# Optimization experiments

Measured on AMD Instinct MI355X. Metric: run time of the kernel, lower is better.

Reference implementation:

```python
import jax, jax.numpy as jnp
import numpy as np

B, TQ, TV, D = 8, 2048, 2048, 128
NEG = 1e9  # keras Attention uses additive -1e9 masking for fp32


def setup_inputs() -> dict:
    key = jax.random.key(0)
    kq, kv, kk, kmq, kmv = jax.random.split(key, 5)
    q = jax.random.normal(kq, (B, TQ, D), dtype=jnp.float32)
    v = jax.random.normal(kv, (B, TV, D), dtype=jnp.float32)
    k = jax.random.normal(kk, (B, TV, D), dtype=jnp.float32)
    # learned scalar scale from use_scale=True, initialized to ones
    scale = jnp.ones((), dtype=jnp.float32)
    mask_q = jax.random.randint(kmq, (B, TQ), 0, 2) > 0
    mask_v = jax.random.randint(kmv, (B, TV), 0, 2) > 0
    return {"q": q, "v": v, "k": k, "scale": scale, "mask_q": mask_q, "mask_v": mask_v}


def reference(q, v, k, scale, mask_q, mask_v):
    # scores: [B, Tq, Tv]
    scores = scale * jnp.einsum('bqd,bkd->bqk', q, k)
    # key/value mask: additive -1e9 on masked positions (keras semantics)
    scores = scores - NEG * (1.0 - mask_v[:, None, :].astype(scores.dtype))
    weights = jax.nn.softmax(scores, axis=-1)
    out = jnp.einsum('bqk,bkd->bqd', weights, v)
    # query mask zeroes out masked query rows
    out = out * mask_q[:, :, None].astype(out.dtype)
    return out
```

## Files before the change

### kernel.cpp

```cpp
#include <hip/hip_runtime.h>
#include <cstddef>

#define NB 8
#define TQ 2048
#define TV 2048
#define DD 128
#define KVT 32
#define NWV 4
#define CHW (TV / NWV)
#define NT  (CHW / KVT)

typedef _Float16 f16x8 __attribute__((ext_vector_type(8)));
typedef _Float16 f16x4 __attribute__((ext_vector_type(4)));
typedef float f32x4 __attribute__((ext_vector_type(4)));

template <int CTRL>
__device__ __forceinline__ float dpp_mov(float x) {
  return __builtin_bit_cast(float,
      __builtin_amdgcn_update_dpp(0, __builtin_bit_cast(int, x), CTRL, 0xF, 0xF, true));
}
__device__ __forceinline__ float rowmax16(float x) {
  x = fmaxf(x, dpp_mov<0x128>(x));
  x = fmaxf(x, dpp_mov<0x124>(x));
  x = fmaxf(x, dpp_mov<0x122>(x));
  x = fmaxf(x, dpp_mov<0x121>(x));
  return x;
}

__global__ __launch_bounds__(256) void prepass_kernel(
    const float* __restrict__ q, const float* __restrict__ k,
    const float* __restrict__ v, const float* __restrict__ scale_p,
    _Float16* __restrict__ qh, _Float16* __restrict__ kh2, _Float16* __restrict__ vt2)
{
  __shared__ _Float16 tlds[32 * 34];
  const int tid = threadIdx.x;
  const int bid = blockIdx.x;
  if (bid < 2048) {
    const float sc = scale_p[0];
    size_t idx = (size_t)bid * 256 + tid;
    float4 x = ((const float4*)q)[idx];
    f16x4 h; h[0] = (_Float16)(sc * x.x); h[1] = (_Float16)(sc * x.y);
    h[2] = (_Float16)(sc * x.z); h[3] = (_Float16)(sc * x.w);
    ((f16x4*)qh)[idx] = h;
  } else if (bid < 2048 + 512) {
    int tb = bid - 2048;
    int b = tb >> 6, kt = tb & 63;
    int row = tid >> 3, d0 = (tid & 7) * 4;
    const float* src = k + ((size_t)(b * TV + kt * 32 + row)) * DD;
    _Float16* dst = kh2 + ((size_t)(b * 64 + kt)) * 4096;
#pragma unroll
    for (int it = 0; it < 4; ++it) {
      float4 x = *(const float4*)(src + it * 32 + d0);
      f16x4 h; h[0] = (_Float16)x.x; h[1] = (_Float16)x.y;
      h[2] = (_Float16)x.z; h[3] = (_Float16)x.w;
      *(f16x4*)(dst + it * 1024 + row * 32 + d0) = h;
    }
  } else {
    int tb = bid - 2048 - 512;
    int b = tb >> 8, rem = tb & 255;
    int kt = rem >> 2, dt = rem & 3;
    int r = tid >> 3, c0 = (tid & 7) * 4;
    float4 x = *(const float4*)&v[((size_t)b * TV + kt * 32 + r) * DD + dt * 32 + c0];
    tlds[(c0 + 0) * 34 + r] = (_Float16)x.x;
    tlds[(c0 + 1) * 34 + r] = (_Float16)x.y;
    tlds[(c0 + 2) * 34 + r] = (_Float16)x.z;
    tlds[(c0 + 3) * 34 + r] = (_Float16)x.w;
    __syncthreads();
    int dl = tid >> 3, k0 = (tid & 7) * 4;
    f16x4 h;
#pragma unroll
    for (int i = 0; i < 4; ++i) h[i] = tlds[dl * 34 + k0 + i];
    size_t eidx = (((size_t)b * 64 + kt) * 128 + (dt * 32 + dl)) * 32 + k0;
    *(f16x4*)&vt2[eidx] = h;
  }
}

__global__ __launch_bounds__(256, 2) void attn_main(
    const _Float16* __restrict__ qh, const _Float16* __restrict__ kh2,
    const _Float16* __restrict__ vt2,
    const int* __restrict__ mask_q, const int* __restrict__ mask_v,
    float* __restrict__ out)
{
  __shared__ __align__(16) _Float16 plds_all[NWV][2][16 * 40];
  __shared__ __align__(16) float osh[32 * 132];
  __shared__ float msh[NWV][32], lsh[NWV][32];

  const int tid = threadIdx.x;
  const int w = tid >> 6;
  const int lane = tid & 63;
  const int l15 = lane & 15, lg = lane >> 4;

  const int b = blockIdx.x & 7;
  const int qg = blockIdx.x >> 3;
  const int qbase = qg * 32;
  const int t0 = w * (NT);

  const _Float16* qhb = qh + ((size_t)b * TQ + qbase) * DD;
  const _Float16* ktiles = kh2 + (size_t)b * 64 * 4096;
  const _Float16* vtiles = vt2 + (size_t)b * 64 * 4096;
  const int* mvb = mask_v + b * TV;

  f16x8 qf[2][4];
#pragma unroll
  for (int rb = 0; rb < 2; ++rb)
#pragma unroll
    for (int kc = 0; kc < 4; ++kc)
      qf[rb][kc] = *(const f16x8*)(qhb + (size_t)(rb * 16 + l15) * DD + kc * 32 + lg * 8);

  f16x8 vones;
#pragma unroll
  for (int j = 0; j < 8; ++j) vones[j] = (_Float16)1.f;

  f32x4 acc[2][8];
  f32x4 accl[2];
#pragma unroll
  for (int rb = 0; rb < 2; ++rb) {
    accl[rb] = (f32x4){0.f, 0.f, 0.f, 0.f};
#pragma unroll
    for (int ct = 0; ct < 8; ++ct) acc[rb][ct] = (f32x4){0.f, 0.f, 0.f, 0.f};
  }
  float m[2][4];
#pragma unroll
  for (int rb = 0; rb < 2; ++rb)
#pragma unroll
    for (int r = 0; r < 4; ++r) m[rb][r] = -3.0e38f;

  for (int t = 0; t < NT; ++t) {
    const int tile = w * NT + t;
    const int kt = tile * KVT;
    const _Float16* ktb = ktiles + (size_t)tile * 4096;
    const _Float16* vtb = vtiles + (size_t)tile * 4096;

    f32x4 s[2][2];
    s[0][0] = (f32x4){0,0,0,0}; s[0][1] = (f32x4){0,0,0,0};
    s[1][0] = (f32x4){0,0,0,0}; s[1][1] = (f32x4){0,0,0,0};
    __builtin_amdgcn_s_setprio(1);
#pragma unroll
    for (int kc = 0; kc < 4; ++kc) {
      f16x8 kf0 = *(const f16x8*)(ktb + kc * 1024 + l15 * 32 + lg * 8);
      f16x8 kf1 = *(const f16x8*)(ktb + kc * 1024 + (16 + l15) * 32 + lg * 8);
      s[0][0] = __builtin_amdgcn_mfma_f32_16x16x32_f16(qf[0][kc], kf0, s[0][0], 0, 0, 0);
      s[1][0] = __builtin_amdgcn_mfma_f32_16x16x32_f16(qf[1][kc], kf0, s[1][0], 0, 0, 0);
      s[0][1] = __builtin_amdgcn_mfma_f32_16x16x32_f16(qf[0][kc], kf1, s[0][1], 0, 0, 0);
      s[1][1] = __builtin_amdgcn_mfma_f32_16x16x32_f16(qf[1][kc], kf1, s[1][1], 0, 0, 0);
    }
    __builtin_amdgcn_s_setprio(0);

    f16x8 vf[8];
#pragma unroll
    for (int ct = 0; ct < 8; ++ct)
      vf[ct] = *(const f16x8*)(vtb + (ct * 16 + l15) * 32 + lg * 8);

    const float a0 = (mvb[kt + l15]      != 0) ? 0.f : -1e9f;
    const float a1 = (mvb[kt + 16 + l15] != 0) ? 0.f : -1e9f;

    f16x8 pa[2];
#pragma unroll
    for (int rb = 0; rb < 2; ++rb) {
      float pmx[4];
      bool grow = false;
#pragma unroll
      for (int r = 0; r < 4; ++r) {
        s[rb][0][r] += a0;
        s[rb][1][r] += a1;
        pmx[r] = rowmax16(fmaxf(s[rb][0][r], s[rb][1][r]));
        grow = grow || (pmx[r] > m[rb][r] + 8.f);
      }
      if (__any(grow)) {
        f32x4 alv;
#pragma unroll
        for (int r = 0; r < 4; ++r) {
          float mn = fmaxf(m[rb][r], pmx[r]);
          alv[r] = __expf(m[rb][r] - mn);
          m[rb][r] = mn;
        }
        accl[rb] *= alv;
#pragma unroll
        for (int ct = 0; ct < 8; ++ct) acc[rb][ct] *= alv;
      }
      _Float16* pl = plds_all[w][rb];
#pragma unroll
      for (int r = 0; r < 4; ++r) {
        float p0 = __expf(s[rb][0][r] - m[rb][r]);
        float p1 = __expf(s[rb][1][r] - m[rb][r]);
        int row = lg * 4 + r;
        pl[row * 40 + l15]      = (_Float16)p0;
        pl[row * 40 + 16 + l15] = (_Float16)p1;
      }
      pa[rb] = *(const f16x8*)(pl + l15 * 40 + lg * 8);
    }

    __builtin_amdgcn_s_setprio(1);
#pragma unroll
    for (int ct = 0; ct < 8; ++ct) {
      acc[0][ct] = __builtin_amdgcn_mfma_f32_16x16x32_f16(pa[0], vf[ct], acc[0][ct], 0, 0, 0);
      acc[1][ct] = __builtin_amdgcn_mfma_f32_16x16x32_f16(pa[1], vf[ct], acc[1][ct], 0, 0, 0);
    }
    accl[0] = __builtin_amdgcn_mfma_f32_16x16x32_f16(pa[0], vones, accl[0], 0, 0, 0);
    accl[1] = __builtin_amdgcn_mfma_f32_16x16x32_f16(pa[1], vones, accl[1], 0, 0, 0);
    __builtin_amdgcn_s_setprio(0);
  }

  if (l15 == 0) {
#pragma unroll
    for (int rb = 0; rb < 2; ++rb)
#pragma unroll
      for (int r = 0; r < 4; ++r) {
        msh[w][rb * 16 + lg * 4 + r] = m[rb][r];
        lsh[w][rb * 16 + lg * 4 + r] = accl[rb][r];
      }
  }
  __syncthreads();

  float coef[2][4];
#pragma unroll
  for (int rb = 0; rb < 2; ++rb)
#pragma unroll
    for (int r = 0; r < 4; ++r) {
      int row = rb * 16 + lg * 4 + r;
      float mstar = msh[0][row];
#pragma unroll
      for (int wv = 1; wv < NWV; ++wv) mstar = fmaxf(mstar, msh[wv][row]);
      coef[rb][r] = __expf(m[rb][r] - mstar);
    }

#pragma unroll
  for (int wv = 0; wv < NWV; ++wv) {
    if (w == wv) {
#pragma unroll
      for (int rb = 0; rb < 2; ++rb)
#pragma unroll
        for (int ct = 0; ct < 8; ++ct)
#pragma unroll
          for (int r = 0; r < 4; ++r) {
            int idx = (rb * 16 + lg * 4 + r) * 132 + ct * 16 + l15;
            float val = coef[rb][r] * acc[rb][ct][r];
            if (wv == 0) osh[idx] = val; else osh[idx] += val;
          }
    }
    __syncthreads();
  }

  {
    const int row = tid >> 3;
    const int cg = (tid & 7) * 16;
    float mstar = msh[0][row];
#pragma unroll
    for (int wv = 1; wv < NWV; ++wv) mstar = fmaxf(mstar, msh[wv][row]);
    float lstar = 0.f;
#pragma unroll
    for (int wv = 0; wv < NWV; ++wv)
      lstar += __expf(msh[wv][row] - mstar) * lsh[wv][row];
    const int qr = qbase + row;
    const float f = ((mask_q[(size_t)b * TQ + qr] != 0) ? 1.f : 0.f) / lstar;
    float* orow = out + ((size_t)b * TQ + qr) * DD + cg;
#pragma unroll
    for (int i4 = 0; i4 < 4; ++i4) {
      float4 p = *(float4*)&osh[row * 132 + cg + i4 * 4];
      float4 o; o.x = p.x * f; o.y = p.y * f; o.z = p.z * f; o.w = p.w * f;
      *(float4*)(orow + i4 * 4) = o;
    }
  }
}

__global__ __launch_bounds__(64, 4) void attn_f32_kernel(
    const float* __restrict__ q, const float* __restrict__ v,
    const float* __restrict__ k, const float* __restrict__ scale_p,
    const int* __restrict__ mask_q, const int* __restrict__ mask_v,
    float* __restrict__ out)
{
  __shared__ __align__(16) _Float16 plds[16 * 40];
  const int lane = threadIdx.x & 63;
  const int l15 = lane & 15, lg = lane >> 4;
  const int qblocks = TQ / 16;
  const int b = blockIdx.x / qblocks, qb = blockIdx.x % qblocks;
  const int qbase = qb * 16;
  const float scale = scale_p[0];
  const float* qp = q + ((size_t)b * TQ + qbase) * DD;
  const float* kbase = k + (size_t)b * TV * DD;
  const float* vbase = v + (size_t)b * TV * DD;
  const int* mvb = mask_v + b * TV;
  f16x8 qf[4];
#pragma unroll
  for (int kc = 0; kc < 4; ++kc) {
    float4 a = *(const float4*)(qp + (size_t)l15 * DD + kc * 32 + lg * 8);
    float4 bb = *(const float4*)(qp + (size_t)l15 * DD + kc * 32 + lg * 8 + 4);
    f16x8 h; h[0]=(_Float16)a.x;h[1]=(_Float16)a.y;h[2]=(_Float16)a.z;h[3]=(_Float16)a.w;
    h[4]=(_Float16)bb.x;h[5]=(_Float16)bb.y;h[6]=(_Float16)bb.z;h[7]=(_Float16)bb.w;
    qf[kc]=h;
  }
  f32x4 acc[8];
#pragma unroll
  for (int i = 0; i < 8; ++i) acc[i] = (f32x4){0.f,0.f,0.f,0.f};
  float m[4], lsum[4];
#pragma unroll
  for (int r = 0; r < 4; ++r) { m[r] = -3.0e38f; lsum[r] = 0.f; }
  for (int kt = 0; kt < TV; kt += KVT) {
    f32x4 s0 = {0,0,0,0}, s1 = {0,0,0,0};
#pragma unroll
    for (int kc = 0; kc < 4; ++kc) {
      const float* kp0 = kbase + (size_t)(kt + l15) * DD + kc * 32 + lg * 8;
      float4 a = *(const float4*)kp0; float4 bb = *(const float4*)(kp0 + 4);
      f16x8 kf0; kf0[0]=(_Float16)a.x;kf0[1]=(_Float16)a.y;kf0[2]=(_Float16)a.z;kf0[3]=(_Float16)a.w;
      kf0[4]=(_Float16)bb.x;kf0[5]=(_Float16)bb.y;kf0[6]=(_Float16)bb.z;kf0[7]=(_Float16)bb.w;
      s0 = __builtin_amdgcn_mfma_f32_16x16x32_f16(qf[kc], kf0, s0, 0, 0, 0);
      const float* kp1 = kbase + (size_t)(kt + 16 + l15) * DD + kc * 32 + lg * 8;
      a = *(const float4*)kp1; bb = *(const float4*)(kp1 + 4);
      f16x8 kf1; kf1[0]=(_Float16)a.x;kf1[1]=(_Float16)a.y;kf1[2]=(_Float16)a.z;kf1[3]=(_Float16)a.w;
      kf1[4]=(_Float16)bb.x;kf1[5]=(_Float16)bb.y;kf1[6]=(_Float16)bb.z;kf1[7]=(_Float16)bb.w;
      s1 = __builtin_amdgcn_mfma_f32_16x16x32_f16(qf[kc], kf1, s1, 0, 0, 0);
    }
    const float a0 = (mvb[kt + l15] != 0) ? 0.f : -1e9f;
    const float a1 = (mvb[kt + 16 + l15] != 0) ? 0.f : -1e9f;
    float pmx[4];
#pragma unroll
    for (int r = 0; r < 4; ++r) {
      s0[r] = s0[r] * scale + a0; s1[r] = s1[r] * scale + a1;
      pmx[r] = fmaxf(s0[r], s1[r]);
    }
#pragma unroll
    for (int off = 1; off < 16; off <<= 1)
#pragma unroll
      for (int r = 0; r < 4; ++r) pmx[r] = fmaxf(pmx[r], __shfl_xor(pmx[r], off, 64));
    float al[4], ps[4];
#pragma unroll
    for (int r = 0; r < 4; ++r) {
      float mn = fmaxf(m[r], pmx[r]);
      al[r] = __expf(m[r] - mn); m[r] = mn;
      float p0 = __expf(s0[r] - mn), p1 = __expf(s1[r] - mn);
      ps[r] = p0 + p1;
      int row = lg * 4 + r;
      plds[row * 40 + l15] = (_Float16)p0;
      plds[row * 40 + 16 + l15] = (_Float16)p1;
    }
#pragma unroll
    for (int off = 1; off < 16; off <<= 1)
#pragma unroll
      for (int r = 0; r < 4; ++r) ps[r] += __shfl_xor(ps[r], off, 64);
#pragma unroll
    for (int r = 0; r < 4; ++r) {
      lsum[r] = lsum[r] * al[r] + ps[r];
#pragma unroll
      for (int ct = 0; ct < 8; ++ct) acc[ct][r] *= al[r];
    }
    f16x8 pa = *(const f16x8*)&plds[l15 * 40 + lg * 8];
#pragma unroll
    for (int ct = 0; ct < 8; ++ct) {
      const float* vp = vbase + (size_t)(kt + lg * 8) * DD + ct * 16 + l15;
      f16x8 vfx;
#pragma unroll
      for (int j = 0; j < 8; ++j) vfx[j] = (_Float16)vp[(size_t)j * DD];
      acc[ct] = __builtin_amdgcn_mfma_f32_16x16x32_f16(pa, vfx, acc[ct], 0, 0, 0);
    }
  }
  const int* mqb = mask_q + b * TQ;
#pragma unroll
  for (int r = 0; r < 4; ++r) {
    int row = lg * 4 + r;
    int qr = qbase + row;
    float f = ((mqb[qr] != 0) ? 1.f : 0.f) / lsum[r];
    float* orow = out + ((size_t)b * TQ + qr) * DD;
#pragma unroll
    for (int ct = 0; ct < 8; ++ct) orow[ct * 16 + l15] = acc[ct][r] * f;
  }
}

extern "C" void kernel_launch(void* const* d_in, const int* in_sizes, int n_in,
                              void* d_out, int out_size, void* d_ws, size_t ws_size,
                              hipStream_t stream) {
  const float* q      = (const float*)d_in[0];
  const float* v      = (const float*)d_in[1];
  const float* k      = (const float*)d_in[2];
  const float* scale  = (const float*)d_in[3];
  const int*   mask_q = (const int*)d_in[4];
  const int*   mask_v = (const int*)d_in[5];
  float* out = (float*)d_out;

  const size_t need = 3ull * NB * TV * DD * sizeof(_Float16);
  if (ws_size >= need) {
    _Float16* qh  = (_Float16*)d_ws;
    _Float16* kh2 = qh + (size_t)NB * TQ * DD;
    _Float16* vt2 = kh2 + (size_t)NB * TV * DD;
    hipLaunchKernelGGL(prepass_kernel, dim3(2048 + 512 + 2048), dim3(256), 0, stream,
                       q, k, v, scale, qh, kh2, vt2);
    hipLaunchKernelGGL(attn_main, dim3(NB * (TQ / 32)), dim3(256), 0, stream,
                       qh, kh2, vt2, mask_q, mask_v, out);
  } else {
    hipLaunchKernelGGL(attn_f32_kernel, dim3(NB * (TQ / 16)), dim3(64), 0, stream,
                       q, v, k, scale, mask_q, mask_v, out);
  }
}
```

Baseline: 57.30 us.

## Process KV tiles in pairs with batched loads and interleaved QK/softmax/PV

Restructures the per-wave KV loop to handle two tiles per iteration. All K, V and mask loads for both tiles are issued up front, and both QK MFMA blocks run before the two softmax and PV stages. This gives more memory latency hiding and instruction-level parallelism. The row-max DPP reduction now runs only inside the rescale branch, and the P LDS buffer is double-buffered so the two tiles do not conflict. The cost is much higher register pressure from holding 32 fragment vectors, which under launch_bounds(256,2) could cause spills.

```diff
diff --git a/kernel.cpp b/kernel.cpp
--- a/kernel.cpp
+++ b/kernel.cpp
@@ -81,7 +81,7 @@
     const int* __restrict__ mask_q, const int* __restrict__ mask_v,
     float* __restrict__ out)
 {
-  __shared__ __align__(16) _Float16 plds_all[NWV][2][16 * 40];
+  __shared__ __align__(16) _Float16 plds_all[NWV][2][2][16 * 40];
   __shared__ __align__(16) float osh[32 * 132];
   __shared__ float msh[NWV][32], lsh[NWV][32];
 
@@ -93,7 +93,6 @@
   const int b = blockIdx.x & 7;
   const int qg = blockIdx.x >> 3;
   const int qbase = qg * 32;
-  const int t0 = w * (NT);
 
   const _Float16* qhb = qh + ((size_t)b * TQ + qbase) * DD;
   const _Float16* ktiles = kh2 + (size_t)b * 64 * 4096;
@@ -125,52 +124,54 @@
 #pragma unroll
     for (int r = 0; r < 4; ++r) m[rb][r] = -3.0e38f;
 
-  for (int t = 0; t < NT; ++t) {
-    const int tile = w * NT + t;
-    const int kt = tile * KVT;
+  const int tbase = w * NT;
+
+  auto load_k = [&](int tile, f16x8 (&kf)[8]) {
     const _Float16* ktb = ktiles + (size_t)tile * 4096;
+#pragma unroll
+    for (int kc = 0; kc < 4; ++kc) {
+      kf[2 * kc]     = *(const f16x8*)(ktb + kc * 1024 + l15 * 32 + lg * 8);
+      kf[2 * kc + 1] = *(const f16x8*)(ktb + kc * 1024 + (16 + l15) * 32 + lg * 8);
+    }
+  };
+  auto load_v = [&](int tile, f16x8 (&vf)[8]) {
     const _Float16* vtb = vtiles + (size_t)tile * 4096;
-
-    f32x4 s[2][2];
+#pragma unroll
+    for (int ct = 0; ct < 8; ++ct)
+      vf[ct] = *(const f16x8*)(vtb + (ct * 16 + l15) * 32 + lg * 8);
+  };
+  auto do_qk = [&](f16x8 (&kf)[8], f32x4 (&s)[2][2]) {
     s[0][0] = (f32x4){0,0,0,0}; s[0][1] = (f32x4){0,0,0,0};
     s[1][0] = (f32x4){0,0,0,0}; s[1][1] = (f32x4){0,0,0,0};
     __builtin_amdgcn_s_setprio(1);
 #pragma unroll
     for (int kc = 0; kc < 4; ++kc) {
-      f16x8 kf0 = *(const f16x8*)(ktb + kc * 1024 + l15 * 32 + lg * 8);
-      f16x8 kf1 = *(const f16x8*)(ktb + kc * 1024 + (16 + l15) * 32 + lg * 8);
-      s[0][0] = __builtin_amdgcn_mfma_f32_16x16x32_f16(qf[0][kc], kf0, s[0][0], 0, 0, 0);
-      s[1][0] = __builtin_amdgcn_mfma_f32_16x16x32_f16(qf[1][kc], kf0, s[1][0], 0, 0, 0);
-      s[0][1] = __builtin_amdgcn_mfma_f32_16x16x32_f16(qf[0][kc], kf1, s[0][1], 0, 0, 0);
-      s[1][1] = __builtin_amdgcn_mfma_f32_16x16x32_f16(qf[1][kc], kf1, s[1][1], 0, 0, 0);
+      s[0][0] = __builtin_amdgcn_mfma_f32_16x16x32_f16(qf[0][kc], kf[2*kc],   s[0][0], 0, 0, 0);
+      s[1][0] = __builtin_amdgcn_mfma_f32_16x16x32_f16(qf[1][kc], kf[2*kc],   s[1][0], 0, 0, 0);
+      s[0][1] = __builtin_amdgcn_mfma_f32_16x16x32_f16(qf[0][kc], kf[2*kc+1], s[0][1], 0, 0, 0);
+      s[1][1] = __builtin_amdgcn_mfma_f32_16x16x32_f16(qf[1][kc], kf[2*kc+1], s[1][1], 0, 0, 0);
     }
     __builtin_amdgcn_s_setprio(0);
-
-    f16x8 vf[8];
-#pragma unroll
-    for (int ct = 0; ct < 8; ++ct)
-      vf[ct] = *(const f16x8*)(vtb + (ct * 16 + l15) * 32 + lg * 8);
-
-    const float a0 = (mvb[kt + l15]      != 0) ? 0.f : -1e9f;
-    const float a1 = (mvb[kt + 16 + l15] != 0) ? 0.f : -1e9f;
-
-    f16x8 pa[2];
+  };
+  auto do_sm = [&](f32x4 (&s)[2][2], float a0, float a1, int par, f16x8 (&pa)[2]) {
 #pragma unroll
     for (int rb = 0; rb < 2; ++rb) {
-      float pmx[4];
+      _Float16* pl = plds_all[w][par][rb];
+      float plm[4];
       bool grow = false;
 #pragma unroll
       for (int r = 0; r < 4; ++r) {
         s[rb][0][r] += a0;
         s[rb][1][r] += a1;
-        pmx[r] = rowmax16(fmaxf(s[rb][0][r], s[rb][1][r]));
-        grow = grow || (pmx[r] > m[rb][r] + 8.f);
+        plm[r] = fmaxf(s[rb][0][r], s[rb][1][r]);
+        grow = grow || (plm[r] > m[rb][r] + 8.f);
       }
       if (__any(grow)) {
         f32x4 alv;
 #pragma unroll
         for (int r = 0; r < 4; ++r) {
-          float mn = fmaxf(m[rb][r], pmx[r]);
+          float pmx = rowmax16(plm[r]);
+          float mn = fmaxf(m[rb][r], pmx);
           alv[r] = __expf(m[rb][r] - mn);
           m[rb][r] = mn;
         }
@@ -178,7 +179,6 @@
 #pragma unroll
         for (int ct = 0; ct < 8; ++ct) acc[rb][ct] *= alv;
       }
-      _Float16* pl = plds_all[w][rb];
 #pragma unroll
       for (int r = 0; r < 4; ++r) {
         float p0 = __expf(s[rb][0][r] - m[rb][r]);
@@ -189,7 +189,8 @@
       }
       pa[rb] = *(const f16x8*)(pl + l15 * 40 + lg * 8);
     }
-
+  };
+  auto do_pv = [&](f16x8 (&pa)[2], f16x8 (&vf)[8]) {
     __builtin_amdgcn_s_setprio(1);
 #pragma unroll
     for (int ct = 0; ct < 8; ++ct) {
@@ -199,6 +200,34 @@
     accl[0] = __builtin_amdgcn_mfma_f32_16x16x32_f16(pa[0], vones, accl[0], 0, 0, 0);
     accl[1] = __builtin_amdgcn_mfma_f32_16x16x32_f16(pa[1], vones, accl[1], 0, 0, 0);
     __builtin_amdgcn_s_setprio(0);
+  };
+
+#pragma unroll
+  for (int tp = 0; tp < NT / 2; ++tp) {
+    const int tileA = tbase + 2 * tp;
+    const int tileB = tileA + 1;
+    const int mA0i = mvb[tileA * KVT + l15];
+    const int mA1i = mvb[tileA * KVT + 16 + l15];
+    const int mB0i = mvb[tileB * KVT + l15];
+    const int mB1i = mvb[tileB * KVT + 16 + l15];
+    f16x8 kA[8], vA[8], kB[8], vB[8];
+    load_k(tileA, kA);
+    load_v(tileA, vA);
+    load_k(tileB, kB);
+    load_v(tileB, vB);
+    const float aA0 = mA0i ? 0.f : -1e9f;
+    const float aA1 = mA1i ? 0.f : -1e9f;
+    const float aB0 = mB0i ? 0.f : -1e9f;
+    const float aB1 = mB1i ? 0.f : -1e9f;
+
+    f32x4 sA[2][2], sB[2][2];
+    f16x8 paA[2], paB[2];
+    do_qk(kA, sA);
+    do_qk(kB, sB);
+    do_sm(sA, aA0, aA1, 0, paA);
+    do_pv(paA, vA);
+    do_sm(sB, aB0, aB1, 1, paB);
+    do_pv(paB, vB);
   }
 
   if (l15 == 0) {
```

Result: slower. 74.69 us (+30.4%).
